# Kernel optimization log

Measured on AMD Instinct MI355X. Metric: run time of the kernel, lower is better.

The kernel has to match this reference:

```python
import jax, jax.numpy as jnp
import numpy as np

N = 50000      # nodes (== nbr_nodes)
E = 800000     # edges
D_IN = 128
D_H = 128
D_OUT = 47
NOISE_RATE = 0.1
EPS = 1e-12


def _lin_init(key, out_f, in_f):
    # rough Glorot-style init for a PyG Linear weight [out_f, in_f]
    s = 1.0 / np.sqrt(in_f)
    return jax.random.uniform(key, (out_f, in_f), jnp.float32, -s, s)


def setup_inputs() -> dict:
    key = jax.random.key(0)
    ks = jax.random.split(key, 13)
    inp = {
        "x": jax.random.normal(ks[0], (N, D_IN), jnp.float32),
        "edge_index": jax.random.randint(ks[1], (2, E), 0, N, dtype=jnp.int32),
        "noise": jax.random.normal(ks[2], (N, D_IN), jnp.float32),
        # layer 0: in -> hidden
        "W_l0": _lin_init(ks[3], D_H, D_IN),
        "b_l0": jnp.zeros((D_H,), jnp.float32),
        "W_r0": _lin_init(ks[4], D_H, D_IN),
        # layer 1: hidden -> hidden
        "W_l1": _lin_init(ks[5], D_H, D_H),
        "b_l1": jnp.zeros((D_H,), jnp.float32),
        "W_r1": _lin_init(ks[6], D_H, D_H),
        # layer 2: hidden -> out
        "W_l2": _lin_init(ks[7], D_OUT, D_H),
        "b_l2": jnp.zeros((D_OUT,), jnp.float32),
        "W_r2": _lin_init(ks[8], D_OUT, D_H),
    }
    return inp


def _sage_conv(x, src, dst, W_l, b_l, W_r):
    # PyG SAGEConv with mean aggregation:
    #   out_i = W_l @ mean_{j in N(i)} x_j + b_l + W_r @ x_i
    msg = x[src]                                              # [E, d] gather
    ssum = jax.ops.segment_sum(msg, dst, num_segments=N)      # [N, d]
    cnt = jax.ops.segment_sum(jnp.ones((src.shape[0], 1), x.dtype), dst,
                              num_segments=N)                 # [N, 1]
    agg = ssum / jnp.maximum(cnt, 1.0)                        # mean; 0 for isolated nodes
    return agg @ W_l.T + b_l + x @ W_r.T


def _branch(x, src, dst, params):
    # stacked SAGEConv; relu after all but last layer; dropout is identity (eval mode)
    h = None
    n_layers = len(params)
    for i, (W_l, b_l, W_r) in enumerate(params):
        x = _sage_conv(x, src, dst, W_l, b_l, W_r)
        if i != n_layers - 1:
            x = jax.nn.relu(x)
            h = x
    return h, jax.nn.log_softmax(x, axis=1), x


def _add_noise(x, noise):
    # n_id=None path: x + sign(x) * F.normalize(noise, dim=1) * noise_rate
    norm = jnp.sqrt(jnp.sum(noise * noise, axis=1, keepdims=True))
    unit = noise / jnp.maximum(norm, EPS)
    return x + jnp.sign(x) * unit * NOISE_RATE


def reference(x, edge_index, noise,
              W_l0, b_l0, W_r0, W_l1, b_l1, W_r1, W_l2, b_l2, W_r2):
    src, dst = edge_index[0], edge_index[1]
    params = [(W_l0, b_l0, W_r0), (W_l1, b_l1, W_r1), (W_l2, b_l2, W_r2)]
    h_p, y_p, z_p = _branch(x, src, dst, params)
    h_n, y_n, z_n = _branch(_add_noise(x, noise), src, dst, params)
    return (h_p, y_p, z_p, h_n, y_n, z_n)
```

## Files before the change

### kernel.cpp

```cpp
#include <hip/hip_runtime.h>
#include <math.h>


typedef unsigned int uint;
typedef unsigned short ushort;
typedef unsigned char uchar;
typedef short bf16x8 __attribute__((ext_vector_type(8)));
typedef float f32x4 __attribute__((ext_vector_type(4)));

__device__ __forceinline__ ushort f2b(float f) {
  union { float f; uint u; } v; v.f = f;
  uint u = v.u;
  return (ushort)((u + 0x7FFFu + ((u >> 16) & 1u)) >> 16);
}
__device__ __forceinline__ float b2f_lo(uint u) {
  union { uint u; float f; } v; v.u = u << 16; return v.f;
}
__device__ __forceinline__ float b2f_hi(uint u) {
  union { uint u; float f; } v; v.u = u & 0xFFFF0000u; return v.f;
}

#if __has_builtin(__builtin_amdgcn_cvt_f32_fp8)
__device__ __forceinline__ float dec8_0(uint u) { return __builtin_amdgcn_cvt_f32_fp8(u, 0); }
__device__ __forceinline__ float dec8_1(uint u) { return __builtin_amdgcn_cvt_f32_fp8(u, 1); }
__device__ __forceinline__ float dec8_2(uint u) { return __builtin_amdgcn_cvt_f32_fp8(u, 2); }
__device__ __forceinline__ float dec8_3(uint u) { return __builtin_amdgcn_cvt_f32_fp8(u, 3); }
#else
__device__ __forceinline__ float dec8_b(uint b) {
  uint s = (b >> 7) & 1u, ex = (b >> 3) & 0xFu, m = b & 7u;
  union { uint u; float f; } v;
  if (ex == 0) {
    v.f = (float)m * 0.001953125f;
    v.u |= s << 31;
    return v.f;
  }
  v.u = (s << 31) | ((ex + 120u) << 23) | (m << 20);
  return v.f;
}
__device__ __forceinline__ float dec8_0(uint u) { return dec8_b(u & 0xFFu); }
__device__ __forceinline__ float dec8_1(uint u) { return dec8_b((u >> 8) & 0xFFu); }
__device__ __forceinline__ float dec8_2(uint u) { return dec8_b((u >> 16) & 0xFFu); }
__device__ __forceinline__ float dec8_3(uint u) { return dec8_b((u >> 24) & 0xFFu); }
#endif

#if __has_builtin(__builtin_amdgcn_cvt_pk_fp8_f32)
__device__ __forceinline__ uchar enc8(float f) {
  return (uchar)(__builtin_amdgcn_cvt_pk_fp8_f32(f, f, 0u, false) & 0xFFu);
}
#else
__device__ __forceinline__ uchar enc8(float f) {
  union { float f; uint u; } v; v.f = f;
  uint s = v.u >> 31;
  uint a = v.u & 0x7FFFFFFFu;
  if (a >= 0x43E00000u) return (uchar)((s << 7) | 0x7Eu);
  if (a < 0x3C800000u) {
    float q = fabsf(f) * 512.0f;
    uint m = (uint)(q + 0.5f);
    return (uchar)((s << 7) | m);
  }
  uint r = a + 0x00080000u;
  if (r >= 0x43E00000u) return (uchar)((s << 7) | 0x7Eu);
  uint ex = (r >> 23) - 120u;
  uint m = (r >> 20) & 7u;
  return (uchar)((s << 7) | (ex << 3) | m);
}
#endif

__global__ __launch_bounds__(256) void prep_kernel(
    const float* __restrict__ x, const float* __restrict__ noise,
    ushort* __restrict__ XB,
    const float* __restrict__ Wl0, const float* __restrict__ Wr0,
    const float* __restrict__ Wl1, const float* __restrict__ Wr1,
    const float* __restrict__ Wl2, const float* __restrict__ Wr2,
    ushort* __restrict__ WB0, ushort* __restrict__ WB1,
    ushort* __restrict__ WB2, int* __restrict__ cnt, int N) {
  int blk = blockIdx.x, t = threadIdx.x;
  if (blk < 64) {
    int i = blk * 256 + t;
    WB0[i] = f2b(Wl0[i]);
    WB0[16384 + i] = f2b(Wr0[i]);
    WB1[i] = f2b(Wl1[i]);
    WB1[16384 + i] = f2b(Wr1[i]);
    if (i < 6016) {
      WB2[i] = f2b(Wl2[i]);
      WB2[6016 + i] = f2b(Wr2[i]);
    }
  }
  {
    int i = blk * 256 + t;
    if (i < N) cnt[i] = 0;
  }
  int node = (blk * 256 + t) >> 6;
  int lane = t & 63;
  if (node >= N) return;
  size_t base = (size_t)node * 128 + 2 * lane;
  float2 nz = *(const float2*)(noise + base);
  float ss = nz.x * nz.x + nz.y * nz.y;
#pragma unroll
  for (int m = 1; m < 64; m <<= 1) ss += __shfl_xor(ss, m, 64);
  float scale = 0.1f / fmaxf(sqrtf(ss), 1e-12f);
  float2 xv = *(const float2*)(x + base);
  float s0 = (xv.x > 0.f) ? 1.f : ((xv.x < 0.f) ? -1.f : 0.f);
  float s1 = (xv.y > 0.f) ? 1.f : ((xv.y < 0.f) ? -1.f : 0.f);
  float n0 = xv.x + s0 * nz.x * scale;
  float n1 = xv.y + s1 * nz.y * scale;
  uint pc = ((uint)f2b(xv.y) << 16) | f2b(xv.x);
  uint pn = ((uint)f2b(n1) << 16) | f2b(n0);
  *(uint*)(XB + (size_t)(2 * node) * 128 + 2 * lane) = pc;
  *(uint*)(XB + (size_t)(2 * node + 1) * 128 + 2 * lane) = pn;
}

__global__ __launch_bounds__(256) void count_kernel(
    const int* __restrict__ dst, int* __restrict__ cnt,
    int* __restrict__ rank, int E) {
  int e = blockIdx.x * blockDim.x + threadIdx.x;
  if (e >= E) return;
  rank[e] = atomicAdd(&cnt[dst[e]], 1);
}

__global__ __launch_bounds__(256) void scan_blocks(
    const int* __restrict__ cnt, int* __restrict__ loc,
    int* __restrict__ bsum, int n) {
  __shared__ int ls[4];
  int t = threadIdx.x;
  int base = blockIdx.x * 1024 + t * 4;
  int v[4];
  int s = 0;
#pragma unroll
  for (int i = 0; i < 4; ++i) {
    v[i] = (base + i < n) ? cnt[base + i] : 0;
    s += v[i];
  }
  int lane = t & 63, wid = t >> 6;
  int ps = s;
#pragma unroll
  for (int d = 1; d < 64; d <<= 1) {
    int o = __shfl_up(ps, d, 64);
    if (lane >= d) ps += o;
  }
  if (lane == 63) ls[wid] = ps;
  __syncthreads();
  if (t == 0) {
    int r = 0;
#pragma unroll
    for (int w = 0; w < 4; ++w) { int x = ls[w]; ls[w] = r; r += x; }
  }
  __syncthreads();
  int run = ps - s + ls[wid];
#pragma unroll
  for (int i = 0; i < 4; ++i) {
    if (base + i < n) loc[base + i] = run;
    run += v[i];
  }
  if (t == 255) bsum[blockIdx.x] = ps + ls[wid];
}

__global__ __launch_bounds__(256) void scan_apply(
    const int* __restrict__ loc, const int* __restrict__ bsum,
    int* __restrict__ off, int n, int E, int nb) {
  __shared__ int ls[4];
  __shared__ int ex[256];
  int t = threadIdx.x;
  int v = (t < nb) ? bsum[t] : 0;
  int lane = t & 63, wid = t >> 6;
  int ps = v;
#pragma unroll
  for (int d = 1; d < 64; d <<= 1) {
    int o = __shfl_up(ps, d, 64);
    if (lane >= d) ps += o;
  }
  if (lane == 63) ls[wid] = ps;
  __syncthreads();
  if (t == 0) {
    int r = 0;
#pragma unroll
    for (int w = 0; w < 4; ++w) { int x = ls[w]; ls[w] = r; r += x; }
  }
  __syncthreads();
  ex[t] = ps - v + ls[wid];
  __syncthreads();
  int i = blockIdx.x * 256 + t;
  if (i < n) off[i] = loc[i] + ex[i >> 10];
  if (i == 0) off[n] = E;
}

__global__ __launch_bounds__(256) void fill_kernel(
    const int* __restrict__ src, const int* __restrict__ dst,
    const int* __restrict__ rank, const int* __restrict__ off,
    int* __restrict__ csr, int E) {
  int e = blockIdx.x * blockDim.x + threadIdx.x;
  if (e >= E) return;
  csr[off[dst[e]] + rank[e]] = src[e];
}

__global__ __launch_bounds__(512) void gemm_fused(
    const ushort* __restrict__ A, const ushort* __restrict__ W,
    uchar* __restrict__ P8, ushort* __restrict__ Rb, int M) {
  __shared__ ushort As[128 * 72];
  __shared__ ushort Ws[256 * 72];
  int tid = threadIdx.x;
  int lane = tid & 63, wid = tid >> 6;
  int wm = wid & 1, wn = wid >> 1;
  int lrow = lane & 15, quad = lane >> 4;
  int row0 = blockIdx.x * 128;

  f32x4 acc[4][4];
#pragma unroll
  for (int mt = 0; mt < 4; ++mt)
#pragma unroll
    for (int nt = 0; nt < 4; ++nt) acc[mt][nt] = (f32x4)(0.f);

  for (int k0 = 0; k0 < 128; k0 += 64) {
    for (int c = tid; c < 128 * 8; c += 512) {
      int r = c >> 3, kc = c & 7;
      int gr = row0 + r;
      uint4 v = make_uint4(0, 0, 0, 0);
      if (gr < M) v = *(const uint4*)(A + (size_t)gr * 128 + k0 + kc * 8);
      *(uint4*)(As + r * 72 + kc * 8) = v;
    }
    for (int c = tid; c < 256 * 8; c += 512) {
      int r = c >> 3, kc = c & 7;
      uint4 v = *(const uint4*)(W + (size_t)r * 128 + k0 + kc * 8);
      *(uint4*)(Ws + r * 72 + kc * 8) = v;
    }
    __syncthreads();
#pragma unroll
    for (int ks = 0; ks < 64; ks += 32) {
      bf16x8 af[4], bw[4];
#pragma unroll
      for (int mt = 0; mt < 4; ++mt)
        af[mt] = *(const bf16x8*)(As + (wm * 64 + mt * 16 + lrow) * 72 + ks + quad * 8);
#pragma unroll
      for (int nt = 0; nt < 4; ++nt)
        bw[nt] = *(const bf16x8*)(Ws + (wn * 64 + nt * 16 + lrow) * 72 + ks + quad * 8);
#pragma unroll
      for (int mt = 0; mt < 4; ++mt)
#pragma unroll
        for (int nt = 0; nt < 4; ++nt)
          acc[mt][nt] = __builtin_amdgcn_mfma_f32_16x16x32_bf16(
              af[mt], bw[nt], acc[mt][nt], 0, 0, 0);
    }
    __syncthreads();
  }
  if (wn < 2) {
#pragma unroll
    for (int mt = 0; mt < 4; ++mt) {
#pragma unroll
      for (int nt = 0; nt < 4; ++nt) {
        int col = wn * 64 + nt * 16 + lrow;
#pragma unroll
        for (int rg = 0; rg < 4; rg += 2) {
          int row = row0 + wm * 64 + mt * 16 + quad * 4 + rg;
          if (row >= M) continue;
          int nd = row >> 1;
          float cv = acc[mt][nt][rg];
          float nv = acc[mt][nt][rg + 1];
          uchar c8 = enc8(cv);
          float cr = dec8_0((uint)c8);
          P8[(size_t)nd * 256 + col] = c8;
          P8[(size_t)nd * 256 + 128 + col] = enc8(nv - cr);
        }
      }
    }
  } else {
#pragma unroll
    for (int mt = 0; mt < 4; ++mt) {
#pragma unroll
      for (int nt = 0; nt < 4; ++nt) {
        int colR = (wn - 2) * 64 + nt * 16 + lrow;
#pragma unroll
        for (int rg = 0; rg < 4; ++rg) {
          int row = row0 + wm * 64 + mt * 16 + quad * 4 + rg;
          if (row >= M) continue;
          int nd = row >> 1, hf = row & 1;
          Rb[(size_t)nd * 256 + hf * 128 + colR] = f2b(acc[mt][nt][rg]);
        }
      }
    }
  }
}

__global__ __launch_bounds__(256) void gemm_l2(
    const ushort* __restrict__ A, const ushort* __restrict__ W,
    ushort* __restrict__ Pzc, uchar* __restrict__ Pzd,
    float* __restrict__ Rz, int M) {
  constexpr int NT = 3;
  __shared__ ushort As[128 * 72];
  __shared__ ushort Ws[96 * 72];
  int tid = threadIdx.x;
  int lane = tid & 63, wid = tid >> 6;
  int wm = wid & 1, wn = wid >> 1;
  int lrow = lane & 15, quad = lane >> 4;
  int row0 = blockIdx.x * 128;

  f32x4 acc[4][NT];
#pragma unroll
  for (int mt = 0; mt < 4; ++mt)
#pragma unroll
    for (int nt = 0; nt < NT; ++nt) acc[mt][nt] = (f32x4)(0.f);

  for (int k0 = 0; k0 < 128; k0 += 64) {
    for (int c = tid; c < 128 * 8; c += 256) {
      int r = c >> 3, kc = c & 7;
      int gr = row0 + r;
      uint4 v = make_uint4(0, 0, 0, 0);
      if (gr < M) v = *(const uint4*)(A + (size_t)gr * 128 + k0 + kc * 8);
      *(uint4*)(As + r * 72 + kc * 8) = v;
    }
    for (int c = tid; c < 96 * 8; c += 256) {
      int r = c >> 3, kc = c & 7;
      uint4 v = make_uint4(0, 0, 0, 0);
      if (r < 94) v = *(const uint4*)(W + (size_t)r * 128 + k0 + kc * 8);
      *(uint4*)(Ws + r * 72 + kc * 8) = v;
    }
    __syncthreads();
#pragma unroll
    for (int ks = 0; ks < 64; ks += 32) {
      bf16x8 af[4], bw[NT];
#pragma unroll
      for (int mt = 0; mt < 4; ++mt)
        af[mt] = *(const bf16x8*)(As + (wm * 64 + mt * 16 + lrow) * 72 + ks + quad * 8);
#pragma unroll
      for (int nt = 0; nt < NT; ++nt)
        bw[nt] = *(const bf16x8*)(Ws + (wn * NT * 16 + nt * 16 + lrow) * 72 + ks + quad * 8);
#pragma unroll
      for (int mt = 0; mt < 4; ++mt)
#pragma unroll
        for (int nt = 0; nt < NT; ++nt)
          acc[mt][nt] = __builtin_amdgcn_mfma_f32_16x16x32_bf16(
              af[mt], bw[nt], acc[mt][nt], 0, 0, 0);
    }
    __syncthreads();
  }
#pragma unroll
  for (int mt = 0; mt < 4; ++mt) {
#pragma unroll
    for (int nt = 0; nt < NT; ++nt) {
      int col = wn * NT * 16 + nt * 16 + lrow;
#pragma unroll
      for (int rg = 0; rg < 4; rg += 2) {
        int row = row0 + wm * 64 + mt * 16 + quad * 4 + rg;
        if (row >= M) continue;
        int nd = row >> 1;
        float cv = acc[mt][nt][rg];
        float nv = acc[mt][nt][rg + 1];
        if (col < 47) {
          ushort cb = f2b(cv);
          Pzc[(size_t)nd * 64 + col] = cb;
          Pzd[(size_t)nd * 64 + col] = enc8(nv - b2f_lo((uint)cb));
        } else if (col < 94) {
          Rz[(size_t)nd * 96 + (col - 47)] = cv;
          Rz[(size_t)nd * 96 + 48 + (col - 47)] = nv;
        }
      }
    }
  }
}

template <bool WF32>
__global__ __launch_bounds__(256) void agg_dual128(
    const uchar* __restrict__ P8, const ushort* __restrict__ Rb,
    const float* __restrict__ bias, const int* __restrict__ off,
    const int* __restrict__ csr, float* __restrict__ f0,
    float* __restrict__ f1, ushort* __restrict__ bout, int N) {
  int node = (blockIdx.x * blockDim.x + threadIdx.x) >> 6;
  int lane = threadIdx.x & 63;
  if (node >= N) return;
  int lq = lane & 31;
  int b = off[node], e = off[node + 1];
  float s0 = 0.f, s1 = 0.f, s2 = 0.f, s3 = 0.f;
  float t0 = 0.f, t1 = 0.f, t2 = 0.f, t3 = 0.f;
  int j = b;
  for (; j + 16 <= e; j += 16) {
    int a0 = csr[j],      a1 = csr[j + 1],  a2 = csr[j + 2],  a3 = csr[j + 3];
    int a4 = csr[j + 4],  a5 = csr[j + 5],  a6 = csr[j + 6],  a7 = csr[j + 7];
    int a8 = csr[j + 8],  a9 = csr[j + 9],  aA = csr[j + 10], aB = csr[j + 11];
    int aC = csr[j + 12], aD = csr[j + 13], aE = csr[j + 14], aF = csr[j + 15];
    uint u0 = *(const uint*)(P8 + (size_t)a0 * 256 + 4 * lane);
    uint u1 = *(const uint*)(P8 + (size_t)a1 * 256 + 4 * lane);
    uint u2 = *(const uint*)(P8 + (size_t)a2 * 256 + 4 * lane);
    uint u3 = *(const uint*)(P8 + (size_t)a3 * 256 + 4 * lane);
    uint u4 = *(const uint*)(P8 + (size_t)a4 * 256 + 4 * lane);
    uint u5 = *(const uint*)(P8 + (size_t)a5 * 256 + 4 * lane);
    uint u6 = *(const uint*)(P8 + (size_t)a6 * 256 + 4 * lane);
    uint u7 = *(const uint*)(P8 + (size_t)a7 * 256 + 4 * lane);
    uint v0 = *(const uint*)(P8 + (size_t)a8 * 256 + 4 * lane);
    uint v1 = *(const uint*)(P8 + (size_t)a9 * 256 + 4 * lane);
    uint v2 = *(const uint*)(P8 + (size_t)aA * 256 + 4 * lane);
    uint v3 = *(const uint*)(P8 + (size_t)aB * 256 + 4 * lane);
    uint v4 = *(const uint*)(P8 + (size_t)aC * 256 + 4 * lane);
    uint v5 = *(const uint*)(P8 + (size_t)aD * 256 + 4 * lane);
    uint v6 = *(const uint*)(P8 + (size_t)aE * 256 + 4 * lane);
    uint v7 = *(const uint*)(P8 + (size_t)aF * 256 + 4 * lane);
    s0 += dec8_0(u0) + dec8_0(u1) + dec8_0(u2) + dec8_0(u3);
    s1 += dec8_1(u0) + dec8_1(u1) + dec8_1(u2) + dec8_1(u3);
    s2 += dec8_2(u0) + dec8_2(u1) + dec8_2(u2) + dec8_2(u3);
    s3 += dec8_3(u0) + dec8_3(u1) + dec8_3(u2) + dec8_3(u3);
    t0 += dec8_0(u4) + dec8_0(u5) + dec8_0(u6) + dec8_0(u7);
    t1 += dec8_1(u4) + dec8_1(u5) + dec8_1(u6) + dec8_1(u7);
    t2 += dec8_2(u4) + dec8_2(u5) + dec8_2(u6) + dec8_2(u7);
    t3 += dec8_3(u4) + dec8_3(u5) + dec8_3(u6) + dec8_3(u7);
    s0 += dec8_0(v0) + dec8_0(v1) + dec8_0(v2) + dec8_0(v3);
    s1 += dec8_1(v0) + dec8_1(v1) + dec8_1(v2) + dec8_1(v3);
    s2 += dec8_2(v0) + dec8_2(v1) + dec8_2(v2) + dec8_2(v3);
    s3 += dec8_3(v0) + dec8_3(v1) + dec8_3(v2) + dec8_3(v3);
    t0 += dec8_0(v4) + dec8_0(v5) + dec8_0(v6) + dec8_0(v7);
    t1 += dec8_1(v4) + dec8_1(v5) + dec8_1(v6) + dec8_1(v7);
    t2 += dec8_2(v4) + dec8_2(v5) + dec8_2(v6) + dec8_2(v7);
    t3 += dec8_3(v4) + dec8_3(v5) + dec8_3(v6) + dec8_3(v7);
  }
  if (j + 8 <= e) {
    int a0 = csr[j],     a1 = csr[j + 1], a2 = csr[j + 2], a3 = csr[j + 3];
    int a4 = csr[j + 4], a5 = csr[j + 5], a6 = csr[j + 6], a7 = csr[j + 7];
    uint u0 = *(const uint*)(P8 + (size_t)a0 * 256 + 4 * lane);
    uint u1 = *(const uint*)(P8 + (size_t)a1 * 256 + 4 * lane);
    uint u2 = *(const uint*)(P8 + (size_t)a2 * 256 + 4 * lane);
    uint u3 = *(const uint*)(P8 + (size_t)a3 * 256 + 4 * lane);
    uint u4 = *(const uint*)(P8 + (size_t)a4 * 256 + 4 * lane);
    uint u5 = *(const uint*)(P8 + (size_t)a5 * 256 + 4 * lane);
    uint u6 = *(const uint*)(P8 + (size_t)a6 * 256 + 4 * lane);
    uint u7 = *(const uint*)(P8 + (size_t)a7 * 256 + 4 * lane);
    s0 += dec8_0(u0) + dec8_0(u1) + dec8_0(u2) + dec8_0(u3);
    s1 += dec8_1(u0) + dec8_1(u1) + dec8_1(u2) + dec8_1(u3);
    s2 += dec8_2(u0) + dec8_2(u1) + dec8_2(u2) + dec8_2(u3);
    s3 += dec8_3(u0) + dec8_3(u1) + dec8_3(u2) + dec8_3(u3);
    t0 += dec8_0(u4) + dec8_0(u5) + dec8_0(u6) + dec8_0(u7);
    t1 += dec8_1(u4) + dec8_1(u5) + dec8_1(u6) + dec8_1(u7);
    t2 += dec8_2(u4) + dec8_2(u5) + dec8_2(u6) + dec8_2(u7);
    t3 += dec8_3(u4) + dec8_3(u5) + dec8_3(u6) + dec8_3(u7);
    j += 8;
  }
  if (j + 4 <= e) {
    int a0 = csr[j], a1 = csr[j + 1], a2 = csr[j + 2], a3 = csr[j + 3];
    uint u0 = *(const uint*)(P8 + (size_t)a0 * 256 + 4 * lane);
    uint u1 = *(const uint*)(P8 + (size_t)a1 * 256 + 4 * lane);
    uint u2 = *(const uint*)(P8 + (size_t)a2 * 256 + 4 * lane);
    uint u3 = *(const uint*)(P8 + (size_t)a3 * 256 + 4 * lane);
    s0 += dec8_0(u0) + dec8_0(u1) + dec8_0(u2) + dec8_0(u3);
    s1 += dec8_1(u0) + dec8_1(u1) + dec8_1(u2) + dec8_1(u3);
    s2 += dec8_2(u0) + dec8_2(u1) + dec8_2(u2) + dec8_2(u3);
    s3 += dec8_3(u0) + dec8_3(u1) + dec8_3(u2) + dec8_3(u3);
    j += 4;
  }
  for (; j < e; ++j) {
    uint u0 = *(const uint*)(P8 + (size_t)csr[j] * 256 + 4 * lane);
    s0 += dec8_0(u0);
    s1 += dec8_1(u0);
    s2 += dec8_2(u0);
    s3 += dec8_3(u0);
  }
  s0 += t0; s1 += t1; s2 += t2; s3 += t3;
  float o0 = __shfl_xor(s0, 32, 64);
  float o1 = __shfl_xor(s1, 32, 64);
  float o2 = __shfl_xor(s2, 32, 64);
  float o3 = __shfl_xor(s3, 32, 64);
  bool hi = lane >= 32;
  float m0 = hi ? (s0 + o0) : s0;
  float m1 = hi ? (s1 + o1) : s1;
  float m2 = hi ? (s2 + o2) : s2;
  float m3 = hi ? (s3 + o3) : s3;
  float invd = 1.f / (float)max(e - b, 1);
  uint2 rp = *(const uint2*)(Rb + (size_t)node * 256 + 4 * lane);
  float rvx = b2f_lo(rp.x), rvy = b2f_hi(rp.x);
  float rvz = b2f_lo(rp.y), rvw = b2f_hi(rp.y);
  float4 bb = *(const float4*)(bias + 4 * lq);
  float q0 = fmaxf(m0 * invd + bb.x + rvx, 0.f);
  float q1 = fmaxf(m1 * invd + bb.y + rvy, 0.f);
  float q2 = fmaxf(m2 * invd + bb.z + rvz, 0.f);
  float q3 = fmaxf(m3 * invd + bb.w + rvw, 0.f);
  size_t arow = (size_t)(2 * node + (hi ? 1 : 0)) * 128 + 4 * lq;
  ushort4 pk;
  pk.x = f2b(q0); pk.y = f2b(q1); pk.z = f2b(q2); pk.w = f2b(q3);
  *(ushort4*)(bout + arow) = pk;
  if (WF32) {
    float* dst = (hi ? f1 : f0) + (size_t)node * 128 + 4 * lq;
    *(float4*)dst = make_float4(q0, q1, q2, q3);
  }
}

__global__ __launch_bounds__(256) void agg47_dual(
    const ushort* __restrict__ Pzc, const uchar* __restrict__ Pzd,
    const float* __restrict__ Rz, const float* __restrict__ bias,
    const int* __restrict__ off, const int* __restrict__ csr,
    float* __restrict__ z0, float* __restrict__ z1, float* __restrict__ y0,
    float* __restrict__ y1, int N) {
  int node = (blockIdx.x * blockDim.x + threadIdx.x) >> 6;
  int lane = threadIdx.x & 63;
  if (node >= N) return;
  int lq = lane & 31;
  bool hiH = lane >= 32;
  int b = off[node], e = off[node + 1];
  float c0s = 0.f, c1s = 0.f;
  float c2s = 0.f, c3s = 0.f;
  float g0 = 0.f, g1 = 0.f;
  float h0 = 0.f, h1 = 0.f;
  int j = b;
  for (; j + 16 <= e; j += 16) {
    int a0 = csr[j],      a1 = csr[j + 1],  a2 = csr[j + 2],  a3 = csr[j + 3];
    int a4 = csr[j + 4],  a5 = csr[j + 5],  a6 = csr[j + 6],  a7 = csr[j + 7];
    int a8 = csr[j + 8],  a9 = csr[j + 9],  aA = csr[j + 10], aB = csr[j + 11];
    int aC = csr[j + 12], aD = csr[j + 13], aE = csr[j + 14], aF = csr[j + 15];
    int p0 = hiH ? a1 : a0;
    int p1 = hiH ? a3 : a2;
    int p2 = hiH ? a5 : a4;
    int p3 = hiH ? a7 : a6;
    int p4 = hiH ? a9 : a8;
    int p5 = hiH ? aB : aA;
    int p6 = hiH ? aD : aC;
    int p7 = hiH ? aF : aE;
    uint c0 = *(const uint*)(Pzc + (size_t)p0 * 64 + 2 * lq);
    uint c1 = *(const uint*)(Pzc + (size_t)p1 * 64 + 2 * lq);
    uint c2 = *(const uint*)(Pzc + (size_t)p2 * 64 + 2 * lq);
    uint c3 = *(const uint*)(Pzc + (size_t)p3 * 64 + 2 * lq);
    uint c4 = *(const uint*)(Pzc + (size_t)p4 * 64 + 2 * lq);
    uint c5 = *(const uint*)(Pzc + (size_t)p5 * 64 + 2 * lq);
    uint c6 = *(const uint*)(Pzc + (size_t)p6 * 64 + 2 * lq);
    uint c7 = *(const uint*)(Pzc + (size_t)p7 * 64 + 2 * lq);
    uint d0 = *(const ushort*)(Pzd + (size_t)p0 * 64 + 2 * lq);
    uint d1 = *(const ushort*)(Pzd + (size_t)p1 * 64 + 2 * lq);
    uint d2 = *(const ushort*)(Pzd + (size_t)p2 * 64 + 2 * lq);
    uint d3 = *(const ushort*)(Pzd + (size_t)p3 * 64 + 2 * lq);
    uint d4 = *(const ushort*)(Pzd + (size_t)p4 * 64 + 2 * lq);
    uint d5 = *(const ushort*)(Pzd + (size_t)p5 * 64 + 2 * lq);
    uint d6 = *(const ushort*)(Pzd + (size_t)p6 * 64 + 2 * lq);
    uint d7 = *(const ushort*)(Pzd + (size_t)p7 * 64 + 2 * lq);
    c0s += b2f_lo(c0) + b2f_lo(c1) + b2f_lo(c2) + b2f_lo(c3);
    c1s += b2f_hi(c0) + b2f_hi(c1) + b2f_hi(c2) + b2f_hi(c3);
    c2s += b2f_lo(c4) + b2f_lo(c5) + b2f_lo(c6) + b2f_lo(c7);
    c3s += b2f_hi(c4) + b2f_hi(c5) + b2f_hi(c6) + b2f_hi(c7);
    g0 += dec8_0(d0) + dec8_0(d1) + dec8_0(d2) + dec8_0(d3);
    g1 += dec8_1(d0) + dec8_1(d1) + dec8_1(d2) + dec8_1(d3);
    h0 += dec8_0(d4) + dec8_0(d5) + dec8_0(d6) + dec8_0(d7);
    h1 += dec8_1(d4) + dec8_1(d5) + dec8_1(d6) + dec8_1(d7);
  }
  if (j + 8 <= e) {
    int a0 = csr[j],     a1 = csr[j + 1], a2 = csr[j + 2], a3 = csr[j + 3];
    int a4 = csr[j + 4], a5 = csr[j + 5], a6 = csr[j + 6], a7 = csr[j + 7];
    int p0 = hiH ? a1 : a0;
    int p1 = hiH ? a3 : a2;
    int p2 = hiH ? a5 : a4;
    int p3 = hiH ? a7 : a6;
    uint c0 = *(const uint*)(Pzc + (size_t)p0 * 64 + 2 * lq);
    uint c1 = *(const uint*)(Pzc + (size_t)p1 * 64 + 2 * lq);
    uint c2 = *(const uint*)(Pzc + (size_t)p2 * 64 + 2 * lq);
    uint c3 = *(const uint*)(Pzc + (size_t)p3 * 64 + 2 * lq);
    uint d0 = *(const ushort*)(Pzd + (size_t)p0 * 64 + 2 * lq);
    uint d1 = *(const ushort*)(Pzd + (size_t)p1 * 64 + 2 * lq);
    uint d2 = *(const ushort*)(Pzd + (size_t)p2 * 64 + 2 * lq);
    uint d3 = *(const ushort*)(Pzd + (size_t)p3 * 64 + 2 * lq);
    c0s += b2f_lo(c0) + b2f_lo(c1) + b2f_lo(c2) + b2f_lo(c3);
    c1s += b2f_hi(c0) + b2f_hi(c1) + b2f_hi(c2) + b2f_hi(c3);
    g0 += dec8_0(d0) + dec8_0(d1) + dec8_0(d2) + dec8_0(d3);
    g1 += dec8_1(d0) + dec8_1(d1) + dec8_1(d2) + dec8_1(d3);
    j += 8;
  }
  if (j + 4 <= e) {
    int a0 = csr[j], a1 = csr[j + 1], a2 = csr[j + 2], a3 = csr[j + 3];
    int p0 = hiH ? a1 : a0;
    int p1 = hiH ? a3 : a2;
    uint c0 = *(const uint*)(Pzc + (size_t)p0 * 64 + 2 * lq);
    uint c1 = *(const uint*)(Pzc + (size_t)p1 * 64 + 2 * lq);
    uint d0 = *(const ushort*)(Pzd + (size_t)p0 * 64 + 2 * lq);
    uint d1 = *(const ushort*)(Pzd + (size_t)p1 * 64 + 2 * lq);
    c0s += b2f_lo(c0) + b2f_lo(c1);
    c1s += b2f_hi(c0) + b2f_hi(c1);
    g0 += dec8_0(d0) + dec8_0(d1);
    g1 += dec8_1(d0) + dec8_1(d1);
    j += 2 * 2;
  }
  if (j + 2 <= e) {
    int a0 = csr[j], a1 = csr[j + 1];
    int p0 = hiH ? a1 : a0;
    uint c0 = *(const uint*)(Pzc + (size_t)p0 * 64 + 2 * lq);
    uint d0 = *(const ushort*)(Pzd + (size_t)p0 * 64 + 2 * lq);
    c0s += b2f_lo(c0);
    c1s += b2f_hi(c0);
    g0 += dec8_0(d0);
    g1 += dec8_1(d0);
    j += 2;
  }
  if (j < e) {
    int a0 = csr[j];
    if (!hiH) {
      uint c0 = *(const uint*)(Pzc + (size_t)a0 * 64 + 2 * lq);
      uint d0 = *(const ushort*)(Pzd + (size_t)a0 * 64 + 2 * lq);
      c0s += b2f_lo(c0);
      c1s += b2f_hi(c0);
      g0 += dec8_0(d0);
      g1 += dec8_1(d0);
    }
  }
  c0s += c2s; c1s += c3s; g0 += h0; g1 += h1;
  c0s += __shfl_xor(c0s, 32, 64);
  c1s += __shfl_xor(c1s, 32, 64);
  g0 += __shfl_xor(g0, 32, 64);
  g1 += __shfl_xor(g1, 32, 64);
  float cc0 = __shfl(c0s, lane >> 1, 64);
  float cc1 = __shfl(c1s, lane >> 1, 64);
  float dd0 = __shfl(g0, lane >> 1, 64);
  float dd1 = __shfl(g1, lane >> 1, 64);
  float cl = (lane & 1) ? cc1 : cc0;
  float dl = (lane & 1) ? dd1 : dd0;
  bool v = lane < 47;
  float invd = 1.f / (float)max(e - b, 1);
  float rc = Rz[(size_t)node * 96 + lane];
  float rn = Rz[(size_t)node * 96 + 48 + lane];
  float bl = v ? bias[lane] : 0.f;
  float za = v ? (cl * invd + bl + rc) : -INFINITY;
  float zn = v ? ((cl + dl) * invd + bl + rn) : -INFINITY;
  float ma = za, mb = zn;
#pragma unroll
  for (int d = 1; d < 64; d <<= 1) {
    ma = fmaxf(ma, __shfl_xor(ma, d, 64));
    mb = fmaxf(mb, __shfl_xor(mb, d, 64));
  }
  float sa = v ? __expf(za - ma) : 0.f;
  float sb = v ? __expf(zn - mb) : 0.f;
#pragma unroll
  for (int d = 1; d < 64; d <<= 1) {
    sa += __shfl_xor(sa, d, 64);
    sb += __shfl_xor(sb, d, 64);
  }
  float lsa = logf(sa) + ma;
  float lsb = logf(sb) + mb;
  if (v) {
    z0[(size_t)node * 47 + lane] = za;
    y0[(size_t)node * 47 + lane] = za - lsa;
    z1[(size_t)node * 47 + lane] = zn;
    y1[(size_t)node * 47 + lane] = zn - lsb;
  }
}

extern "C" void kernel_launch(void* const* d_in, const int* in_sizes, int n_in,
                              void* d_out, int out_size, void* d_ws,
                              size_t ws_size, hipStream_t stream) {
  const float* x = (const float*)d_in[0];
  const int* ei = (const int*)d_in[1];
  const float* noise = (const float*)d_in[2];
  const float* Wl0 = (const float*)d_in[3];
  const float* bl0 = (const float*)d_in[4];
  const float* Wr0 = (const float*)d_in[5];
  const float* Wl1 = (const float*)d_in[6];
  const float* bl1 = (const float*)d_in[7];
  const float* Wr1 = (const float*)d_in[8];
  const float* Wl2 = (const float*)d_in[9];
  const float* bl2 = (const float*)d_in[10];
  const float* Wr2 = (const float*)d_in[11];

  const int N = in_sizes[0] / 128;
  const int E = in_sizes[1] / 2;
  const int M = 2 * N;

  float* out = (float*)d_out;
  float* h_p = out;
  float* y_p = h_p + (size_t)N * 128;
  float* z_p = y_p + (size_t)N * 47;
  float* h_n = z_p + (size_t)N * 47;
  float* y_n = h_n + (size_t)N * 128;
  float* z_n = y_n + (size_t)N * 47;

  char* w = (char*)d_ws;
  auto alloc = [&](size_t bytes) {
    void* p = (void*)w;
    w += (bytes + 511) & ~(size_t)511;
    return p;
  };
  ushort* XB = (ushort*)alloc((size_t)M * 128 * 2);
  uchar* P8 = (uchar*)alloc((size_t)N * 256);
  ushort* Rb = (ushort*)alloc((size_t)M * 128 * 2);
  float* Rz = (float*)alloc((size_t)N * 128 * 4);
  ushort* WB0 = (ushort*)alloc(256 * 128 * 2);
  ushort* WB1 = (ushort*)alloc(256 * 128 * 2);
  ushort* WB2 = (ushort*)alloc(94 * 128 * 2);
  int* cnt = (int*)alloc((size_t)N * 4);
  int* off = (int*)alloc((size_t)(N + 1) * 4);
  int* rank = (int*)alloc((size_t)E * 4);
  int* loc = (int*)alloc((size_t)N * 4);
  int* bsum = (int*)alloc((size_t)256 * 4);
  int* csr = (int*)alloc((size_t)E * 4);
  ushort* Pzc = (ushort*)P8;
  uchar* Pzd = P8 + (size_t)N * 128;

  int nwb = (N + 3) / 4;
  int rb = (M + 127) / 128;
  int eb = (E + 255) / 256;
  int sb = (N + 1023) / 1024;

  prep_kernel<<<nwb, 256, 0, stream>>>(x, noise, XB, Wl0, Wr0, Wl1, Wr1, Wl2,
                                       Wr2, WB0, WB1, WB2, cnt, N);

  count_kernel<<<eb, 256, 0, stream>>>(ei + E, cnt, rank, E);
  scan_blocks<<<sb, 256, 0, stream>>>(cnt, loc, bsum, N);
  scan_apply<<<(N + 255) / 256, 256, 0, stream>>>(loc, bsum, off, N, E, sb);
  fill_kernel<<<eb, 256, 0, stream>>>(ei, ei + E, rank, off, csr, E);

  gemm_fused<<<rb, 512, 0, stream>>>(XB, WB0, P8, Rb, M);
  agg_dual128<false><<<nwb, 256, 0, stream>>>(P8, Rb, bl0, off, csr, nullptr,
                                              nullptr, XB, N);
  gemm_fused<<<rb, 512, 0, stream>>>(XB, WB1, P8, Rb, M);
  agg_dual128<true><<<nwb, 256, 0, stream>>>(P8, Rb, bl1, off, csr, h_p, h_n,
                                             XB, N);
  gemm_l2<<<rb, 256, 0, stream>>>(XB, WB2, Pzc, Pzd, Rz, M);
  agg47_dual<<<nwb, 256, 0, stream>>>(Pzc, Pzd, Rz, bl2, off, csr, z_p, z_n,
                                      y_p, y_n, N);
}
```

Baseline: 400.9 us.

## Fold edge counting into prep kernel and CSR fill into first GEMM launch

Edge-degree counting with atomics now runs inside the prep kernel, and the count buffer is zeroed by a memset beforehand. The CSR fill runs as extra trailing blocks of the first layer GEMM launch, so independent work shares one launch. This removes two kernel launches and their serialization gaps. In exchange, the GEMM kernel carries a branch and extra parameters, and its fill blocks compete with GEMM blocks for the GPU.

```diff
diff --git a/kernel.cpp b/kernel.cpp
--- a/kernel.cpp
+++ b/kernel.cpp
@@ -73,7 +73,8 @@
     const float* __restrict__ Wl1, const float* __restrict__ Wr1,
     const float* __restrict__ Wl2, const float* __restrict__ Wr2,
     ushort* __restrict__ WB0, ushort* __restrict__ WB1,
-    ushort* __restrict__ WB2, int* __restrict__ cnt, int N) {
+    ushort* __restrict__ WB2, const int* __restrict__ dst,
+    int* __restrict__ cnt, int* __restrict__ rank, int E, int eb, int N) {
   int blk = blockIdx.x, t = threadIdx.x;
   if (blk < 64) {
     int i = blk * 256 + t;
@@ -86,9 +87,9 @@
       WB2[6016 + i] = f2b(Wr2[i]);
     }
   }
-  {
-    int i = blk * 256 + t;
-    if (i < N) cnt[i] = 0;
+  if (blk < eb) {
+    int e = blk * 256 + t;
+    if (e < E) rank[e] = atomicAdd(&cnt[dst[e]], 1);
   }
   int node = (blk * 256 + t) >> 6;
   int lane = t & 63;
@@ -110,14 +111,6 @@
   *(uint*)(XB + (size_t)(2 * node + 1) * 128 + 2 * lane) = pn;
 }
 
-__global__ __launch_bounds__(256) void count_kernel(
-    const int* __restrict__ dst, int* __restrict__ cnt,
-    int* __restrict__ rank, int E) {
-  int e = blockIdx.x * blockDim.x + threadIdx.x;
-  if (e >= E) return;
-  rank[e] = atomicAdd(&cnt[dst[e]], 1);
-}
-
 __global__ __launch_bounds__(256) void scan_blocks(
     const int* __restrict__ cnt, int* __restrict__ loc,
     int* __restrict__ bsum, int n) {
@@ -184,21 +177,22 @@
   if (i == 0) off[n] = E;
 }
 
-__global__ __launch_bounds__(256) void fill_kernel(
+__global__ __launch_bounds__(512) void gemm_fused(
+    const ushort* __restrict__ A, const ushort* __restrict__ W,
+    uchar* __restrict__ P8, ushort* __restrict__ Rb, int M,
     const int* __restrict__ src, const int* __restrict__ dst,
     const int* __restrict__ rank, const int* __restrict__ off,
-    int* __restrict__ csr, int E) {
-  int e = blockIdx.x * blockDim.x + threadIdx.x;
-  if (e >= E) return;
-  csr[off[dst[e]] + rank[e]] = src[e];
-}
-
-__global__ __launch_bounds__(512) void gemm_fused(
-    const ushort* __restrict__ A, const ushort* __restrict__ W,
-    uchar* __restrict__ P8, ushort* __restrict__ Rb, int M) {
+    int* __restrict__ csr, int E, int rb) {
   __shared__ ushort As[128 * 72];
   __shared__ ushort Ws[256 * 72];
   int tid = threadIdx.x;
+  if (blockIdx.x >= rb) {
+    int base = (blockIdx.x - rb) * 1024 + tid;
+    if (base < E) csr[off[dst[base]] + rank[base]] = src[base];
+    int e1 = base + 512;
+    if (e1 < E) csr[off[dst[e1]] + rank[e1]] = src[e1];
+    return;
+  }
   int lane = tid & 63, wid = tid >> 6;
   int wm = wid & 1, wn = wid >> 1;
   int lrow = lane & 15, quad = lane >> 4;
@@ -566,7 +560,7 @@
     c1s += b2f_hi(c0) + b2f_hi(c1);
     g0 += dec8_0(d0) + dec8_0(d1);
     g1 += dec8_1(d0) + dec8_1(d1);
-    j += 2 * 2;
+    j += 4;
   }
   if (j + 2 <= e) {
     int a0 = csr[j], a1 = csr[j + 1];
@@ -684,20 +678,24 @@
   int nwb = (N + 3) / 4;
   int rb = (M + 127) / 128;
   int eb = (E + 255) / 256;
+  int fb = (E + 1023) / 1024;
   int sb = (N + 1023) / 1024;
 
+  hipMemsetAsync(cnt, 0, (size_t)N * 4, stream);
+
   prep_kernel<<<nwb, 256, 0, stream>>>(x, noise, XB, Wl0, Wr0, Wl1, Wr1, Wl2,
-                                       Wr2, WB0, WB1, WB2, cnt, N);
-
-  count_kernel<<<eb, 256, 0, stream>>>(ei + E, cnt, rank, E);
+                                       Wr2, WB0, WB1, WB2, ei + E, cnt, rank,
+                                       E, eb, N);
+
   scan_blocks<<<sb, 256, 0, stream>>>(cnt, loc, bsum, N);
   scan_apply<<<(N + 255) / 256, 256, 0, stream>>>(loc, bsum, off, N, E, sb);
-  fill_kernel<<<eb, 256, 0, stream>>>(ei, ei + E, rank, off, csr, E);
-
-  gemm_fused<<<rb, 512, 0, stream>>>(XB, WB0, P8, Rb, M);
+
+  gemm_fused<<<rb + fb, 512, 0, stream>>>(XB, WB0, P8, Rb, M, ei, ei + E,
+                                          rank, off, csr, E, rb);
   agg_dual128<false><<<nwb, 256, 0, stream>>>(P8, Rb, bl0, off, csr, nullptr,
                                               nullptr, XB, N);
-  gemm_fused<<<rb, 512, 0, stream>>>(XB, WB1, P8, Rb, M);
+  gemm_fused<<<rb, 512, 0, stream>>>(XB, WB1, P8, Rb, M, ei, ei + E, rank,
+                                     off, csr, E, rb);
   agg_dual128<true><<<nwb, 256, 0, stream>>>(P8, Rb, bl1, off, csr, h_p, h_n,
                                              XB, N);
   gemm_l2<<<rb, 256, 0, stream>>>(XB, WB2, Pzc, Pzd, Rz, M);
```

Result: faster. 384.9 us (-4.0%).
